# Kernel optimization log

Hardware: AMD Instinct MI355X
Metric: run time of the kernel (lower is better)

Reference implementation:

```python
import jax, jax.numpy as jnp
import numpy as np

ROI_SIZE = 5
BOX = 4.0  # hardcoded box_size in the module


def _bilinear(fm_b, y, x):
    """torchvision roi_align bilinear sample. fm_b: [C,H,W]; y,x: [N,P,P].
    Returns [N,C,P,P]."""
    C, H, W = fm_b.shape
    valid = (y > -1.0) & (y < H) & (x > -1.0) & (x < W)
    y = jnp.maximum(y, 0.0)
    x = jnp.maximum(x, 0.0)
    y0 = jnp.floor(y).astype(jnp.int32)
    x0 = jnp.floor(x).astype(jnp.int32)
    yc = y0 >= H - 1
    xc = x0 >= W - 1
    y0 = jnp.where(yc, H - 1, y0)
    x0 = jnp.where(xc, W - 1, x0)
    y1 = jnp.minimum(y0 + 1, H - 1)
    x1 = jnp.minimum(x0 + 1, W - 1)
    ly = jnp.where(yc, 0.0, y - y0)  # torchvision sets y=y_low at the top edge
    lx = jnp.where(xc, 0.0, x - x0)
    hy, hx = 1.0 - ly, 1.0 - lx
    # advanced indexing gathers -> [C,N,P,P]
    v00 = fm_b[:, y0, x0]
    v01 = fm_b[:, y0, x1]
    v10 = fm_b[:, y1, x0]
    v11 = fm_b[:, y1, x1]
    w00 = (hy * hx)[None]
    w01 = (hy * lx)[None]
    w10 = (ly * hx)[None]
    w11 = (ly * lx)[None]
    out = w00 * v00 + w01 * v01 + w10 * v10 + w11 * v11
    out = out * valid[None].astype(fm_b.dtype)
    return jnp.transpose(out, (1, 0, 2, 3))  # [N,C,P,P]


def _roi_align_points(fm_b, cand_b):
    """fm_b: [C,H,W]; cand_b: [N,2] (x,y). One sample per bin (sampling_ratio
    resolves to 1 since ceil(4/5)=1), spatial_scale=1, aligned=False."""
    bin_sz = BOX / ROI_SIZE
    off = (jnp.arange(ROI_SIZE, dtype=fm_b.dtype) + 0.5) * bin_sz  # bin centers
    xs = (cand_b[:, 0] - BOX / 2)[:, None] + off[None, :]  # [N,P]
    ys = (cand_b[:, 1] - BOX / 2)[:, None] + off[None, :]  # [N,P]
    Y = ys[:, :, None] * jnp.ones((1, 1, ROI_SIZE), fm_b.dtype)  # [N,P,P]
    X = xs[:, None, :] * jnp.ones((1, ROI_SIZE, 1), fm_b.dtype)
    Y = jnp.broadcast_to(ys[:, :, None], (ys.shape[0], ROI_SIZE, ROI_SIZE))
    X = jnp.broadcast_to(xs[:, None, :], (xs.shape[0], ROI_SIZE, ROI_SIZE))
    return _bilinear(fm_b, Y, X)  # [N,C,P,P]


def setup_inputs() -> dict:
    key = jax.random.key(0)
    k1, k2 = jax.random.split(key)
    B, C, H, W, N = 8, 256, 135, 240, 1024
    feature_map = jax.random.normal(k1, (B, C, H, W), dtype=jnp.float32)
    # (x, y) points in feature-map coordinates (spatial_scale=1.0)
    candidates = jax.random.uniform(k2, (B, N, 2), dtype=jnp.float32) * jnp.array(
        [W - 1.0, H - 1.0], dtype=jnp.float32
    )
    return {"feature_map": feature_map, "candidates": candidates}


def reference(feature_map, candidates):
    B, C, H, W = feature_map.shape
    N = candidates.shape[1]
    aligned = jax.vmap(_roi_align_points)(feature_map, candidates)  # [B,N,C,P,P]
    return aligned.reshape(B, N, C * ROI_SIZE * ROI_SIZE)
```

## Files before the change

### kernel.cpp

```cpp
#include <hip/hip_runtime.h>
#include <hip/hip_bf16.h>

#define ROI 5
#define NPTS 25
#define CCH 256
#define HH 135
#define WW 240
#define HWP (HH * WW)
#define NB 8
#define NN 1024

__global__ __launch_bounds__(256) void transpose_kernel(const float* __restrict__ fm,
                                                        float* __restrict__ fmT) {
    __shared__ float tile[32][33];
    int b   = blockIdx.z;
    int hw0 = blockIdx.x * 32;
    int c0  = blockIdx.y * 32;
    int tx  = threadIdx.x;
    int ty  = threadIdx.y;

    const float* src = fm + (size_t)b * CCH * HWP;
#pragma unroll
    for (int j = 0; j < 32; j += 8) {
        int hw = hw0 + tx;
        int c  = c0 + ty + j;
        if (hw < HWP) tile[ty + j][tx] = src[(size_t)c * HWP + hw];
    }
    __syncthreads();
    float* dst = fmT + (size_t)b * HWP * CCH;
#pragma unroll
    for (int j = 0; j < 32; j += 8) {
        int hw = hw0 + ty + j;
        int c  = c0 + tx;
        if (hw < HWP) dst[(size_t)hw * CCH + c] = tile[tx][ty + j];
    }
}

template <bool TRANSPOSED>
__global__ __launch_bounds__(256) void roi_kernel(const float* __restrict__ fmsrc,
                                                  const float* __restrict__ cand,
                                                  float* __restrict__ out) {
    __shared__ __align__(16) float res[CCH * NPTS];
    __shared__ int   s_y0[NPTS], s_x0[NPTS], s_y1[NPTS], s_x1[NPTS];
    __shared__ float s_w[4][NPTS];

    int blk = blockIdx.x;
    int b   = blk >> 10;
    int n   = blk & 1023;
    int t   = threadIdx.x;

    float cx = cand[(b * NN + n) * 2 + 0];
    float cy = cand[(b * NN + n) * 2 + 1];

    if (t < NPTS) {
        int py = t / ROI, px = t % ROI;
        float y = (cy - 2.0f) + ((float)py + 0.5f) * 0.8f;
        float x = (cx - 2.0f) + ((float)px + 0.5f) * 0.8f;
        bool valid = (y > -1.0f) && (y < (float)HH) && (x > -1.0f) && (x < (float)WW);
        y = fmaxf(y, 0.0f);
        x = fmaxf(x, 0.0f);
        int y0 = (int)floorf(y);
        int x0 = (int)floorf(x);
        bool yc = (y0 >= HH - 1);
        bool xc = (x0 >= WW - 1);
        if (yc) y0 = HH - 1;
        if (xc) x0 = WW - 1;
        int y1 = min(y0 + 1, HH - 1);
        int x1 = min(x0 + 1, WW - 1);
        float ly = yc ? 0.0f : y - (float)y0;
        float lx = xc ? 0.0f : x - (float)x0;
        float hy = 1.0f - ly, hx = 1.0f - lx;
        float v  = valid ? 1.0f : 0.0f;
        s_y0[t] = y0; s_x0[t] = x0; s_y1[t] = y1; s_x1[t] = x1;
        s_w[0][t] = hy * hx * v;
        s_w[1][t] = hy * lx * v;
        s_w[2][t] = ly * hx * v;
        s_w[3][t] = ly * lx * v;
    }
    __syncthreads();

    int sub  = t >> 6;
    int lane = t & 63;

    for (int p = sub; p < NPTS; p += 4) {
        int y0 = s_y0[p], x0 = s_x0[p], y1 = s_y1[p], x1 = s_x1[p];
        float w00 = s_w[0][p], w01 = s_w[1][p], w10 = s_w[2][p], w11 = s_w[3][p];

        const float *p00, *p01, *p10, *p11;
        size_t cstride;
        if (TRANSPOSED) {
            const float* base = fmsrc + (size_t)b * HWP * CCH;
            p00 = base + (size_t)(y0 * WW + x0) * CCH;
            p01 = base + (size_t)(y0 * WW + x1) * CCH;
            p10 = base + (size_t)(y1 * WW + x0) * CCH;
            p11 = base + (size_t)(y1 * WW + x1) * CCH;
            cstride = 1;
        } else {
            const float* base = fmsrc + (size_t)b * CCH * HWP;
            p00 = base + (y0 * WW + x0);
            p01 = base + (y0 * WW + x1);
            p10 = base + (y1 * WW + x0);
            p11 = base + (y1 * WW + x1);
            cstride = HWP;
        }
#pragma unroll
        for (int i = 0; i < 4; i++) {
            int c = lane + 64 * i;
            size_t co = (size_t)c * cstride;
            float v00 = p00[co], v01 = p01[co], v10 = p10[co], v11 = p11[co];
            res[c * NPTS + p] = w00 * v00 + w01 * v01 + w10 * v10 + w11 * v11;
        }
    }
    __syncthreads();

    float4* o4 = (float4*)(out + (size_t)blk * (CCH * NPTS));
    const float4* r4 = (const float4*)res;
    for (int k = t; k < (CCH * NPTS) / 4; k += 256) {
        o4[k] = r4[k];
    }
}

extern "C" void kernel_launch(void* const* d_in, const int* in_sizes, int n_in,
                              void* d_out, int out_size, void* d_ws, size_t ws_size,
                              hipStream_t stream) {
    const float* fm   = (const float*)d_in[0];
    const float* cand = (const float*)d_in[1];
    float* out        = (float*)d_out;

    size_t needed = (size_t)NB * HWP * CCH * sizeof(float);
    if (ws_size >= needed) {
        float* fmT = (float*)d_ws;
        dim3 tb(32, 8);
        dim3 tg((HWP + 31) / 32, CCH / 32, NB);
        transpose_kernel<<<tg, tb, 0, stream>>>(fm, fmT);
        roi_kernel<true><<<NB * NN, 256, 0, stream>>>(fmT, cand, out);
    } else {
        roi_kernel<false><<<NB * NN, 256, 0, stream>>>(fm, cand, out);
    }
}
```

Measured before the change: 509.2 us.

## Stage each channel plane in LDS as fp16 and gather bilinear samples from LDS

Replaces the transpose-plus-gather pipeline with one kernel that assigns a block to each (batch, channel) plane. The block loads the 135x240 plane once with float4 reads, converts it to half precision so it fits in LDS, and computes all 1024x25 samples for that channel from LDS. This removes the full transposed copy of the feature map and the scattered global gathers. In exchange, output writes become strided by 25 floats across points, fp16 storage adds rounding error relative to the fp32 reference, and floorf is replaced by an int cast on values that are non-negative after clamping.

```diff
diff --git a/kernel.cpp b/kernel.cpp
--- a/kernel.cpp
+++ b/kernel.cpp
@@ -1,5 +1,5 @@
 #include <hip/hip_runtime.h>
-#include <hip/hip_bf16.h>
+#include <hip/hip_fp16.h>
 
 #define ROI 5
 #define NPTS 25
@@ -7,60 +7,53 @@
 #define HH 135
 #define WW 240
 #define HWP (HH * WW)
+#define NV4 (HWP / 4)
 #define NB 8
 #define NN 1024
 
-__global__ __launch_bounds__(256) void transpose_kernel(const float* __restrict__ fm,
-                                                        float* __restrict__ fmT) {
-    __shared__ float tile[32][33];
-    int b   = blockIdx.z;
-    int hw0 = blockIdx.x * 32;
-    int c0  = blockIdx.y * 32;
-    int tx  = threadIdx.x;
-    int ty  = threadIdx.y;
+__global__ __launch_bounds__(1024) void roi_plane_kernel(const float* __restrict__ fm,
+                                                         const float* __restrict__ cand,
+                                                         float* __restrict__ out) {
+    __shared__ __half plane[HWP];
 
-    const float* src = fm + (size_t)b * CCH * HWP;
+    int blk = blockIdx.x;
+    int c   = blk & (CCH - 1);
+    int b   = blk >> 8;
+    int t   = threadIdx.x;
+
+    const float4* src = (const float4*)(fm + ((size_t)b * CCH + c) * HWP);
 #pragma unroll
-    for (int j = 0; j < 32; j += 8) {
-        int hw = hw0 + tx;
-        int c  = c0 + ty + j;
-        if (hw < HWP) tile[ty + j][tx] = src[(size_t)c * HWP + hw];
+    for (int j = 0; j < 8; j++) {
+        int e = j * 1024 + t;
+        if (e < NV4) {
+            float4 v = src[e];
+            __half2* d = (__half2*)(plane + e * 4);
+            d[0] = __half2(__float2half(v.x), __float2half(v.y));
+            d[1] = __half2(__float2half(v.z), __float2half(v.w));
+        }
     }
     __syncthreads();
-    float* dst = fmT + (size_t)b * HWP * CCH;
-#pragma unroll
-    for (int j = 0; j < 32; j += 8) {
-        int hw = hw0 + ty + j;
-        int c  = c0 + tx;
-        if (hw < HWP) dst[(size_t)hw * CCH + c] = tile[tx][ty + j];
-    }
-}
 
-template <bool TRANSPOSED>
-__global__ __launch_bounds__(256) void roi_kernel(const float* __restrict__ fmsrc,
-                                                  const float* __restrict__ cand,
-                                                  float* __restrict__ out) {
-    __shared__ __align__(16) float res[CCH * NPTS];
-    __shared__ int   s_y0[NPTS], s_x0[NPTS], s_y1[NPTS], s_x1[NPTS];
-    __shared__ float s_w[4][NPTS];
+    const float* cb = cand + (size_t)b * NN * 2;
+    float* ob = out + (size_t)b * NN * (CCH * NPTS) + c * NPTS;
 
-    int blk = blockIdx.x;
-    int b   = blk >> 10;
-    int n   = blk & 1023;
-    int t   = threadIdx.x;
+    for (int k = 0; k < NPTS; k++) {
+        int idx = k * 1024 + t;
+        int n   = idx / 25;
+        int p   = idx - n * 25;
+        int py  = p / 5;
+        int px  = p - py * 5;
 
-    float cx = cand[(b * NN + n) * 2 + 0];
-    float cy = cand[(b * NN + n) * 2 + 1];
+        float cx = cb[n * 2 + 0];
+        float cy = cb[n * 2 + 1];
 
-    if (t < NPTS) {
-        int py = t / ROI, px = t % ROI;
         float y = (cy - 2.0f) + ((float)py + 0.5f) * 0.8f;
         float x = (cx - 2.0f) + ((float)px + 0.5f) * 0.8f;
         bool valid = (y > -1.0f) && (y < (float)HH) && (x > -1.0f) && (x < (float)WW);
         y = fmaxf(y, 0.0f);
         x = fmaxf(x, 0.0f);
-        int y0 = (int)floorf(y);
-        int x0 = (int)floorf(x);
+        int y0 = (int)y;
+        int x0 = (int)x;
         bool yc = (y0 >= HH - 1);
         bool xc = (x0 >= WW - 1);
         if (yc) y0 = HH - 1;
@@ -70,53 +63,16 @@
         float ly = yc ? 0.0f : y - (float)y0;
         float lx = xc ? 0.0f : x - (float)x0;
         float hy = 1.0f - ly, hx = 1.0f - lx;
-        float v  = valid ? 1.0f : 0.0f;
-        s_y0[t] = y0; s_x0[t] = x0; s_y1[t] = y1; s_x1[t] = x1;
-        s_w[0][t] = hy * hx * v;
-        s_w[1][t] = hy * lx * v;
-        s_w[2][t] = ly * hx * v;
-        s_w[3][t] = ly * lx * v;
-    }
-    __syncthreads();
+        float vm = valid ? 1.0f : 0.0f;
 
-    int sub  = t >> 6;
-    int lane = t & 63;
+        int r0 = y0 * WW, r1 = y1 * WW;
+        float v00 = __half2float(plane[r0 + x0]);
+        float v01 = __half2float(plane[r0 + x1]);
+        float v10 = __half2float(plane[r1 + x0]);
+        float v11 = __half2float(plane[r1 + x1]);
 
-    for (int p = sub; p < NPTS; p += 4) {
-        int y0 = s_y0[p], x0 = s_x0[p], y1 = s_y1[p], x1 = s_x1[p];
-        float w00 = s_w[0][p], w01 = s_w[1][p], w10 = s_w[2][p], w11 = s_w[3][p];
-
-        const float *p00, *p01, *p10, *p11;
-        size_t cstride;
-        if (TRANSPOSED) {
-            const float* base = fmsrc + (size_t)b * HWP * CCH;
-            p00 = base + (size_t)(y0 * WW + x0) * CCH;
-            p01 = base + (size_t)(y0 * WW + x1) * CCH;
-            p10 = base + (size_t)(y1 * WW + x0) * CCH;
-            p11 = base + (size_t)(y1 * WW + x1) * CCH;
-            cstride = 1;
-        } else {
-            const float* base = fmsrc + (size_t)b * CCH * HWP;
-            p00 = base + (y0 * WW + x0);
-            p01 = base + (y0 * WW + x1);
-            p10 = base + (y1 * WW + x0);
-            p11 = base + (y1 * WW + x1);
-            cstride = HWP;
-        }
-#pragma unroll
-        for (int i = 0; i < 4; i++) {
-            int c = lane + 64 * i;
-            size_t co = (size_t)c * cstride;
-            float v00 = p00[co], v01 = p01[co], v10 = p10[co], v11 = p11[co];
-            res[c * NPTS + p] = w00 * v00 + w01 * v01 + w10 * v10 + w11 * v11;
-        }
-    }
-    __syncthreads();
-
-    float4* o4 = (float4*)(out + (size_t)blk * (CCH * NPTS));
-    const float4* r4 = (const float4*)res;
-    for (int k = t; k < (CCH * NPTS) / 4; k += 256) {
-        o4[k] = r4[k];
+        float r = (hy * hx * v00 + hy * lx * v01 + ly * hx * v10 + ly * lx * v11) * vm;
+        ob[(size_t)n * (CCH * NPTS) + p] = r;
     }
 }
 
@@ -127,14 +83,5 @@
     const float* cand = (const float*)d_in[1];
     float* out        = (float*)d_out;
 
-    size_t needed = (size_t)NB * HWP * CCH * sizeof(float);
-    if (ws_size >= needed) {
-        float* fmT = (float*)d_ws;
-        dim3 tb(32, 8);
-        dim3 tg((HWP + 31) / 32, CCH / 32, NB);
-        transpose_kernel<<<tg, tb, 0, stream>>>(fm, fmT);
-        roi_kernel<true><<<NB * NN, 256, 0, stream>>>(fmT, cand, out);
-    } else {
-        roi_kernel<false><<<NB * NN, 256, 0, stream>>>(fm, cand, out);
-    }
+    roi_plane_kernel<<<NB * CCH, 1024, 0, stream>>>(fm, cand, out);
 }
```

Result: faster. 491.1 us (-3.5%).
